# Optimization experiments

Measured on AMD Instinct MI355X. Metric: run time of the kernel, lower is better.

The kernel has to match this reference:

```python
import jax, jax.numpy as jnp
import numpy as np

N = 50000   # nodes
E = 800000  # edges
H = 128     # hidden_dim
K = 4       # Chebyshev order
EPS_BN = 1e-5
EPS_L2 = 1e-12


def setup_inputs() -> dict:
    key = jax.random.key(0)
    ks = jax.random.split(key, 8)
    x = jax.random.normal(ks[0], (N, 3), dtype=jnp.float32)
    edge_index = jax.random.randint(ks[1], (2, E), 0, N, dtype=jnp.int32)

    def lin(k, fi, fo):
        s = 1.0 / np.sqrt(fi)
        return jax.random.uniform(k, (fi, fo), jnp.float32, -s, s)

    def cheb_params(k, fi, fo):
        kk = jax.random.split(k, K)
        W = jnp.stack([lin(kk[i], fi, fo) for i in range(K)])  # [K, fi, fo]
        b = jnp.zeros((fo,), jnp.float32)
        return W, b

    W1, b1 = cheb_params(ks[2], 3, H)
    W2, b2 = cheb_params(ks[3], H, H)
    W3, b3 = cheb_params(ks[4], H, H)
    W4, b4 = cheb_params(ks[5], H, H)
    Wr = lin(ks[6], H, 3)
    br = jnp.zeros((3,), jnp.float32)
    ones = jnp.ones((H,), jnp.float32)
    zeros = jnp.zeros((H,), jnp.float32)
    return {
        'x': x, 'edge_index': edge_index,
        'W1': W1, 'b1': b1, 'W2': W2, 'b2': b2,
        'W3': W3, 'b3': b3, 'W4': W4, 'b4': b4,
        'g1': ones, 'be1': zeros, 'g2': ones, 'be2': zeros,
        'g3': ones, 'be3': zeros, 'Wr': Wr, 'br': br,
    }


def _prop(h, src, dst, norm):
    # one sparse Laplacian application: out[dst] += norm * h[src]
    return jax.ops.segment_sum(norm[:, None] * h[src], dst, num_segments=N)


def _cheb(h, src, dst, norm, W, b):
    # PyG ChebConv with sym normalization, lambda_max=2 -> L_hat edge weights
    # are -D^-1/2 A D^-1/2 with zero diagonal (encoded in norm).
    out = h @ W[0]
    Tx0, Tx1 = h, _prop(h, src, dst, norm)
    out = out + Tx1 @ W[1]
    for k in range(2, W.shape[0]):
        Tx2 = 2.0 * _prop(Tx1, src, dst, norm) - Tx0
        out = out + Tx2 @ W[k]
        Tx0, Tx1 = Tx1, Tx2
    return out + b


def _bn(h, g, b):
    # BatchNorm1d in training mode: batch stats over node dim, biased var
    m = h.mean(axis=0)
    v = h.var(axis=0)
    return g * (h - m) * jax.lax.rsqrt(v + EPS_BN) + b


def reference(x, edge_index, W1, b1, W2, b2, W3, b3, W4, b4,
              g1, be1, g2, be2, g3, be3, Wr, br):
    src, dst = edge_index[0], edge_index[1]
    deg = jax.ops.segment_sum(jnp.ones((E,), jnp.float32), src, num_segments=N)
    dinv = jnp.where(deg > 0, jax.lax.rsqrt(jnp.maximum(deg, 1.0)), 0.0)
    norm = -dinv[src] * dinv[dst]

    h = _bn(jax.nn.leaky_relu(_cheb(x, src, dst, norm, W1, b1)), g1, be1)
    h = _bn(jax.nn.leaky_relu(_cheb(h, src, dst, norm, W2, b2)), g2, be2)
    h = _bn(jax.nn.relu(_cheb(h, src, dst, norm, W3, b3)), g3, be3)
    h = _cheb(h, src, dst, norm, W4, b4)
    # F.normalize(p=2, dim=1)
    h = h / jnp.maximum(jnp.linalg.norm(h, axis=1, keepdims=True), EPS_L2)
    return h @ Wr + br
```

## Files before the change

### kernel.cpp

```cpp
#include <hip/hip_runtime.h>
#include <hip/hip_fp16.h>

#define HD 128

typedef __attribute__((ext_vector_type(8))) short bf16x8;
typedef __attribute__((ext_vector_type(4))) float f32x4;
typedef unsigned int u32;

struct h4s { __half2 a, b; };

__device__ __forceinline__ float lrelu(float x, float s) { return x > 0.f ? x : s * x; }

__device__ __forceinline__ u32 bf16rtne(float x) {
  u32 u = __float_as_uint(x);
  return (u + 0x7fffu + ((u >> 16) & 1u)) >> 16;
}

__global__ void k_edge_count(const int* __restrict__ src, const int* __restrict__ dst,
                             int* __restrict__ degc, int* __restrict__ cnt,
                             int* __restrict__ ledge, int E) {
  int e = blockIdx.x * blockDim.x + threadIdx.x;
  if (e < E) {
    atomicAdd(&degc[src[e]], 1);
    ledge[e] = atomicAdd(&cnt[dst[e]], 1);
  }
}

__global__ __launch_bounds__(1024) void k_scan1(const int* __restrict__ cnt,
                                                int* __restrict__ rowptr,
                                                int* __restrict__ bsums, int n) {
  __shared__ int buf[1024];
  int i = blockIdx.x * 1024 + threadIdx.x;
  int v = (i < n) ? cnt[i] : 0;
  buf[threadIdx.x] = v;
  __syncthreads();
  for (int o = 1; o < 1024; o <<= 1) {
    int t = (threadIdx.x >= (unsigned)o) ? buf[threadIdx.x - o] : 0;
    __syncthreads();
    buf[threadIdx.x] += t;
    __syncthreads();
  }
  if (i < n) rowptr[i] = buf[threadIdx.x] - v;
  if (threadIdx.x == 1023) bsums[blockIdx.x] = buf[1023];
}

__global__ __launch_bounds__(1024) void k_scan3(int* __restrict__ rowptr,
                                                const int* __restrict__ bsums,
                                                const int* __restrict__ degc,
                                                float* __restrict__ dinv, int n, int Etot,
                                                int nb) {
  __shared__ int blockoff;
  if (nb <= 64) {
    if (threadIdx.x < 64) {
      int lane = threadIdx.x;
      int v = (lane < nb) ? bsums[lane] : 0;
      int inc = v;
#pragma unroll
      for (int o = 1; o < 64; o <<= 1) {
        int t = __shfl_up(inc, o, 64);
        if (lane >= o) inc += t;
      }
      if (lane == (int)blockIdx.x) blockoff = inc - v;
    }
  } else if (threadIdx.x == 0) {
    int sum = 0;
    for (int t = 0; t < (int)blockIdx.x; ++t) sum += bsums[t];
    blockoff = sum;
  }
  __syncthreads();
  int i = blockIdx.x * 1024 + threadIdx.x;
  if (i < n) {
    rowptr[i] += blockoff;
    int dg = degc[i];
    dinv[i] = dg > 0 ? rsqrtf((float)dg) : 0.f;
  }
  if (i == 0) rowptr[n] = Etot;
}

__global__ void k_fill(const int* __restrict__ src, const int* __restrict__ dst,
                       const int* __restrict__ ledge, const int* __restrict__ rowptr,
                       const float* __restrict__ dinv, uint2* __restrict__ cw, int E) {
  int e = blockIdx.x * blockDim.x + threadIdx.x;
  if (e < E) {
    int s = src[e], d = dst[e];
    int p = rowptr[d] + ledge[e];
    cw[p] = make_uint2((u32)s, __float_as_uint(-dinv[s] * dinv[d]));
  }
}

__global__ void k_prop3(const int* __restrict__ rowptr, const uint2* __restrict__ cw,
                        const float* __restrict__ Hs, const float* __restrict__ Sub,
                        float* __restrict__ Out, float scale, int n) {
  int r = blockIdx.x * blockDim.x + threadIdx.x;
  if (r >= n) return;
  int b = rowptr[r], e = rowptr[r + 1];
  float a0 = 0.f, a1 = 0.f, a2 = 0.f;
  for (int j = b; j < e; ++j) {
    uint2 m = cw[j];
    int s = (int)m.x;
    float w = __uint_as_float(m.y);
    a0 = fmaf(w, Hs[s * 3 + 0], a0);
    a1 = fmaf(w, Hs[s * 3 + 1], a1);
    a2 = fmaf(w, Hs[s * 3 + 2], a2);
  }
  float r0 = scale * a0, r1 = scale * a1, r2 = scale * a2;
  if (Sub) { r0 -= Sub[r * 3 + 0]; r1 -= Sub[r * 3 + 1]; r2 -= Sub[r * 3 + 2]; }
  Out[r * 3 + 0] = r0; Out[r * 3 + 1] = r1; Out[r * 3 + 2] = r2;
}

template <int PHI>
__global__ __launch_bounds__(256) void k_prop128(
    const int* __restrict__ rowptr, const uint2* __restrict__ cw,
    const __half* __restrict__ Ph, const __half* __restrict__ Sub,
    __half* __restrict__ Outh, float scale, int n,
    const float* __restrict__ gsc, const float* __restrict__ gsh,
    const float* __restrict__ ssc, const float* __restrict__ ssh, float slope) {
  int r = blockIdx.x * 4 + (int)(threadIdx.x >> 6);
  int lane = threadIdx.x & 63;
  if (r >= n) return;
  int b = rowptr[r], e = rowptr[r + 1];
  int fl = (lane & 31) << 2;
  int half = lane >> 5;
  float ax = 0.f, ay = 0.f, az = 0.f, aw = 0.f, ws = 0.f;
  int j = b;
  for (; j + 7 < e; j += 8) {
    h4s h[4];
    float w[4];
#pragma unroll
    for (int q = 0; q < 4; ++q) {
      int idx = j + 2 * q + half;
      uint2 m = cw[idx];
      w[q] = __uint_as_float(m.y);
      h[q] = *(const h4s*)&Ph[(size_t)m.x * HD + fl];
    }
#pragma unroll
    for (int q = 0; q < 4; ++q) {
      float2 f0 = __half22float2(h[q].a);
      float2 f1 = __half22float2(h[q].b);
      if (PHI) {
        f0.x = lrelu(f0.x, slope); f0.y = lrelu(f0.y, slope);
        f1.x = lrelu(f1.x, slope); f1.y = lrelu(f1.y, slope);
        ws += w[q];
      }
      ax = fmaf(w[q], f0.x, ax);
      ay = fmaf(w[q], f0.y, ay);
      az = fmaf(w[q], f1.x, az);
      aw = fmaf(w[q], f1.y, aw);
    }
  }
  for (; j + 1 < e; j += 2) {
    int idx = j + half;
    uint2 m = cw[idx];
    float w = __uint_as_float(m.y);
    h4s h = *(const h4s*)&Ph[(size_t)m.x * HD + fl];
    float2 f0 = __half22float2(h.a);
    float2 f1 = __half22float2(h.b);
    if (PHI) {
      f0.x = lrelu(f0.x, slope); f0.y = lrelu(f0.y, slope);
      f1.x = lrelu(f1.x, slope); f1.y = lrelu(f1.y, slope);
      ws += w;
    }
    ax = fmaf(w, f0.x, ax);
    ay = fmaf(w, f0.y, ay);
    az = fmaf(w, f1.x, az);
    aw = fmaf(w, f1.y, aw);
  }
  if (j < e && half == 0) {
    uint2 m = cw[j];
    float w = __uint_as_float(m.y);
    h4s h = *(const h4s*)&Ph[(size_t)m.x * HD + fl];
    float2 f0 = __half22float2(h.a);
    float2 f1 = __half22float2(h.b);
    if (PHI) {
      f0.x = lrelu(f0.x, slope); f0.y = lrelu(f0.y, slope);
      f1.x = lrelu(f1.x, slope); f1.y = lrelu(f1.y, slope);
      ws += w;
    }
    ax = fmaf(w, f0.x, ax);
    ay = fmaf(w, f0.y, ay);
    az = fmaf(w, f1.x, az);
    aw = fmaf(w, f1.y, aw);
  }
  ax += __shfl_xor(ax, 32, 64);
  ay += __shfl_xor(ay, 32, 64);
  az += __shfl_xor(az, 32, 64);
  aw += __shfl_xor(aw, 32, 64);
  if (PHI) {
    ws += __shfl_xor(ws, 32, 64);
    float4 g4 = *(const float4*)&gsc[fl];
    float4 s4 = *(const float4*)&gsh[fl];
    ax = fmaf(ax, g4.x, ws * s4.x);
    ay = fmaf(ay, g4.y, ws * s4.y);
    az = fmaf(az, g4.z, ws * s4.z);
    aw = fmaf(aw, g4.w, ws * s4.w);
  }
  float4 o = make_float4(scale * ax, scale * ay, scale * az, scale * aw);
  if (Sub) {
    h4s sh4 = *(const h4s*)&Sub[(size_t)r * HD + fl];
    float2 s0 = __half22float2(sh4.a);
    float2 s1 = __half22float2(sh4.b);
    if (ssc != nullptr) {
      float4 c4 = *(const float4*)&ssc[fl];
      float4 d4 = *(const float4*)&ssh[fl];
      s0.x = fmaf(lrelu(s0.x, slope), c4.x, d4.x);
      s0.y = fmaf(lrelu(s0.y, slope), c4.y, d4.y);
      s1.x = fmaf(lrelu(s1.x, slope), c4.z, d4.z);
      s1.y = fmaf(lrelu(s1.y, slope), c4.w, d4.w);
    }
    o.x -= s0.x; o.y -= s0.y; o.z -= s1.x; o.w -= s1.y;
  }
  if (half == 0) {
    h4s ho;
    ho.a = __float22half2_rn(make_float2(o.x, o.y));
    ho.b = __float22half2_rn(make_float2(o.z, o.w));
    *(h4s*)&Outh[(size_t)r * HD + fl] = ho;
  }
}

__global__ __launch_bounds__(128) void k_l1gemm(
    const float* __restrict__ X, const float* __restrict__ T1, const float* __restrict__ T2,
    const float* __restrict__ T3, const float* __restrict__ W1, const float* __restrict__ b1,
    __half* __restrict__ Outh, float* __restrict__ bnsum, float* __restrict__ bnsq,
    float slope, int n, int rpb) {
  int j = threadIdx.x;
  float w[12];
#pragma unroll
  for (int t = 0; t < 4; ++t)
#pragma unroll
    for (int c = 0; c < 3; ++c) w[t * 3 + c] = W1[(t * 3 + c) * HD + j];
  float bj = b1[j];
  int r0 = blockIdx.x * rpb, r1 = min(r0 + rpb, n);
  float s = 0.f, q = 0.f;
  for (int r = r0; r < r1; ++r) {
    float acc = bj;
#pragma unroll
    for (int c = 0; c < 3; ++c) {
      acc = fmaf(X [r * 3 + c], w[0 + c], acc);
      acc = fmaf(T1[r * 3 + c], w[3 + c], acc);
      acc = fmaf(T2[r * 3 + c], w[6 + c], acc);
      acc = fmaf(T3[r * 3 + c], w[9 + c], acc);
    }
    Outh[(size_t)r * HD + j] = __float2half(acc);
    float a = lrelu(acc, slope);
    s += a;
    q = fmaf(a, a, q);
  }
  atomicAdd(&bnsum[j], s);
  atomicAdd(&bnsq[j], q);
}

__global__ void k_wsplit3(const float* __restrict__ W2, const float* __restrict__ W3,
                          const float* __restrict__ W4, uint4* __restrict__ Whi,
                          uint4* __restrict__ Wlo) {
  int flat = blockIdx.x * 256 + threadIdx.x;
  int wsel = flat >> 13;
  int f = flat & 8191;
  const float* W = (wsel == 0) ? W2 : (wsel == 1) ? W3 : W4;
  int n = f & 127, K8 = f >> 7;
  int chunk = K8 >> 2, g = K8 & 3;
  bf16x8 hv, lv;
#pragma unroll
  for (int i = 0; i < 8; ++i) {
    int k = chunk * 32 + ((i >> 2) << 4) + g * 4 + (i & 3);
    float v = W[(size_t)k * HD + n];
    u32 hb = bf16rtne(v);
    float hf = __uint_as_float(hb << 16);
    u32 lb = bf16rtne(v - hf);
    hv[i] = (short)hb;
    lv[i] = (short)lb;
  }
  int slot = chunk * 512 + (n >> 4) * 64 + g * 16 + (n & 15);
  Whi[wsel * 8192 + slot] = *(uint4*)&hv;
  Wlo[wsel * 8192 + slot] = *(uint4*)&lv;
}

__global__ __launch_bounds__(256) void k_gemm4m(
    const __half* __restrict__ T0, const __half* __restrict__ T1,
    const __half* __restrict__ T2, const __half* __restrict__ T3,
    const uint4* __restrict__ Whi, const uint4* __restrict__ Wlo,
    const float* __restrict__ bias, __half* __restrict__ OUTh,
    float* bnsum, float* bnsq, float stat_slope,
    const float* __restrict__ gsc, const float* __restrict__ gsh, float phi_slope,
    int nrows) {
  __shared__ short sAh[2048], sAl[2048];
  __shared__ short sWh[4096], sWl[4096];
  __shared__ float redS[128], redQ[128];

  int tid = threadIdx.x;
  int lane = tid & 63, w = tid >> 6, wr = w >> 1, wc = w & 1;
  int g = (tid >> 4) & 3;
  int ri = tid & 15;
  int row0 = blockIdx.x * 64;
  int arow = row0 + w * 16 + ri;
  bool aval = arow < nrows;

  f32x4 zero = {0.f, 0.f, 0.f, 0.f};
  f32x4 acc[2][4];
#pragma unroll
  for (int mi = 0; mi < 2; ++mi)
#pragma unroll
    for (int nj = 0; nj < 4; ++nj) acc[mi][nj] = zero;

  if (tid < 128) { redS[tid] = 0.f; redQ[tid] = 0.f; }

  for (int chunk = 0; chunk < 16; ++chunk) {
    const __half* Ts = (chunk < 4) ? T0 : (chunk < 8) ? T1 : (chunk < 12) ? T2 : T3;
    int kc = chunk & 3;
    float vals[8] = {0.f, 0.f, 0.f, 0.f, 0.f, 0.f, 0.f, 0.f};
    if (aval) {
      const __half* ap = Ts + (size_t)arow * HD + kc * 32 + g * 4;
      h4s va = *(const h4s*)ap;
      h4s vb = *(const h4s*)(ap + 16);
      float2 f0 = __half22float2(va.a), f1 = __half22float2(va.b);
      float2 f2 = __half22float2(vb.a), f3 = __half22float2(vb.b);
      vals[0] = f0.x; vals[1] = f0.y; vals[2] = f1.x; vals[3] = f1.y;
      vals[4] = f2.x; vals[5] = f2.y; vals[6] = f3.x; vals[7] = f3.y;
    }
    size_t wbase = (size_t)chunk * 512;
    uint4 wh0 = Whi[wbase + tid], wh1 = Whi[wbase + 256 + tid];
    uint4 wl0 = Wlo[wbase + tid], wl1 = Wlo[wbase + 256 + tid];

    __syncthreads();

    if (gsc != nullptr && chunk < 4) {
#pragma unroll
      for (int i = 0; i < 8; ++i) {
        int f = kc * 32 + g * 4 + (i & 3) + ((i >> 2) << 4);
        vals[i] = fmaf(lrelu(vals[i], phi_slope), gsc[f], gsh[f]);
      }
    }
    bf16x8 hv, lv;
#pragma unroll
    for (int i = 0; i < 8; ++i) {
      u32 hb = bf16rtne(vals[i]);
      float hf = __uint_as_float(hb << 16);
      u32 lb = bf16rtne(vals[i] - hf);
      hv[i] = (short)hb;
      lv[i] = (short)lb;
    }
    *(bf16x8*)&sAh[tid * 8] = hv;
    *(bf16x8*)&sAl[tid * 8] = lv;
    *(uint4*)&sWh[tid * 8] = wh0;
    *(uint4*)&sWh[(256 + tid) * 8] = wh1;
    *(uint4*)&sWl[tid * 8] = wl0;
    *(uint4*)&sWl[(256 + tid) * 8] = wl1;
    __syncthreads();

    bf16x8 ah[2], al[2], bh[4], bl[4];
#pragma unroll
    for (int mi = 0; mi < 2; ++mi) {
      ah[mi] = *(const bf16x8*)&sAh[((wr * 2 + mi) * 64 + lane) * 8];
      al[mi] = *(const bf16x8*)&sAl[((wr * 2 + mi) * 64 + lane) * 8];
    }
#pragma unroll
    for (int nj = 0; nj < 4; ++nj) {
      bh[nj] = *(const bf16x8*)&sWh[((wc * 4 + nj) * 64 + lane) * 8];
      bl[nj] = *(const bf16x8*)&sWl[((wc * 4 + nj) * 64 + lane) * 8];
    }
#pragma unroll
    for (int mi = 0; mi < 2; ++mi)
#pragma unroll
      for (int nj = 0; nj < 4; ++nj) {
        acc[mi][nj] = __builtin_amdgcn_mfma_f32_16x16x32_bf16(ah[mi], bh[nj], acc[mi][nj], 0, 0, 0);
        acc[mi][nj] = __builtin_amdgcn_mfma_f32_16x16x32_bf16(ah[mi], bl[nj], acc[mi][nj], 0, 0, 0);
        acc[mi][nj] = __builtin_amdgcn_mfma_f32_16x16x32_bf16(al[mi], bh[nj], acc[mi][nj], 0, 0, 0);
      }
  }

  int l4 = (lane >> 4) * 4, ni = lane & 15;
  bool stats = (bnsum != nullptr);
#pragma unroll
  for (int nj = 0; nj < 4; ++nj) {
    int c = wc * 64 + nj * 16 + ni;
    float bcol = bias[c];
    float s = 0.f, q = 0.f;
#pragma unroll
    for (int mi = 0; mi < 2; ++mi)
#pragma unroll
      for (int j = 0; j < 4; ++j) {
        int row = row0 + (wr * 2 + mi) * 16 + l4 + j;
        if (row < nrows) {
          float v = acc[mi][nj][j] + bcol;
          OUTh[(size_t)row * HD + c] = __float2half(v);
          if (stats) {
            float a = lrelu(v, stat_slope);
            s += a;
            q = fmaf(a, a, q);
          }
        }
      }
    if (stats) {
      s += __shfl_xor(s, 16, 64);
      s += __shfl_xor(s, 32, 64);
      q += __shfl_xor(q, 16, 64);
      q += __shfl_xor(q, 32, 64);
      if (lane < 16) {
        atomicAdd(&redS[c], s);
        atomicAdd(&redQ[c], q);
      }
    }
  }
  if (stats) {
    __syncthreads();
    if (tid < 128) {
      atomicAdd(&bnsum[tid], redS[tid]);
      atomicAdd(&bnsq[tid], redQ[tid]);
    }
  }
}

__global__ void k_bnfin(const float* __restrict__ bsum, const float* __restrict__ bsq,
                        const float* __restrict__ g, const float* __restrict__ be,
                        float* __restrict__ scaleb, float* __restrict__ shiftb, int n) {
  int f = threadIdx.x;
  if (f < HD) {
    float m = bsum[f] / (float)n;
    float v = bsq[f] / (float)n - m * m;
    float rs = rsqrtf(v + 1e-5f);
    float sc = g[f] * rs;
    scaleb[f] = sc;
    shiftb[f] = be[f] - m * sc;
  }
}

__global__ __launch_bounds__(256) void k_final(const __half* __restrict__ Hb,
                                               const float* __restrict__ Wr,
                                               const float* __restrict__ br,
                                               float* __restrict__ out, int n) {
  int r = blockIdx.x * 4 + (int)(threadIdx.x >> 6);
  int lane = threadIdx.x & 63;
  if (r >= n) return;
  float h0 = __half2float(Hb[(size_t)r * HD + lane]);
  float h1 = __half2float(Hb[(size_t)r * HD + 64 + lane]);
  float ss = h0 * h0 + h1 * h1;
#pragma unroll
  for (int o = 32; o; o >>= 1) ss += __shfl_xor(ss, o, 64);
  float inv = 1.f / fmaxf(sqrtf(ss), 1e-12f);
  h0 *= inv; h1 *= inv;
  float o0 = h0 * Wr[lane * 3 + 0] + h1 * Wr[(64 + lane) * 3 + 0];
  float o1 = h0 * Wr[lane * 3 + 1] + h1 * Wr[(64 + lane) * 3 + 1];
  float o2 = h0 * Wr[lane * 3 + 2] + h1 * Wr[(64 + lane) * 3 + 2];
#pragma unroll
  for (int o = 32; o; o >>= 1) {
    o0 += __shfl_xor(o0, o, 64);
    o1 += __shfl_xor(o1, o, 64);
    o2 += __shfl_xor(o2, o, 64);
  }
  if (lane == 0) {
    out[r * 3 + 0] = o0 + br[0];
    out[r * 3 + 1] = o1 + br[1];
    out[r * 3 + 2] = o2 + br[2];
  }
}

extern "C" void kernel_launch(void* const* d_in, const int* in_sizes, int n_in,
                              void* d_out, int out_size, void* d_ws, size_t ws_size,
                              hipStream_t stream) {
  const float* x  = (const float*)d_in[0];
  const int*   ei = (const int*)d_in[1];
  const float* W1 = (const float*)d_in[2];
  const float* b1 = (const float*)d_in[3];
  const float* W2 = (const float*)d_in[4];
  const float* b2 = (const float*)d_in[5];
  const float* W3 = (const float*)d_in[6];
  const float* b3 = (const float*)d_in[7];
  const float* W4 = (const float*)d_in[8];
  const float* b4 = (const float*)d_in[9];
  const float* g1 = (const float*)d_in[10];
  const float* be1= (const float*)d_in[11];
  const float* g2 = (const float*)d_in[12];
  const float* be2= (const float*)d_in[13];
  const float* g3 = (const float*)d_in[14];
  const float* be3= (const float*)d_in[15];
  const float* Wr = (const float*)d_in[16];
  const float* br = (const float*)d_in[17];

  const int N = in_sizes[0] / 3;
  const int E = in_sizes[1] / 2;
  const int* src = ei;
  const int* dst = ei + E;
  float* out = (float*)d_out;

  char* wp = (char*)d_ws;
  size_t used = 0;
  auto alloc = [&](size_t bytes) -> void* {
    void* p = (void*)(wp + used);
    used += (bytes + 255) & ~(size_t)255;
    return p;
  };
  int*   deg2   = (int*)alloc((size_t)2 * N * 4);
  int*   rowptr = (int*)alloc((size_t)(N + 1) * 4);
  float* dinv   = (float*)alloc((size_t)N * 4);
  int*   bsums  = (int*)alloc(256 * 4);
  int*   ledge  = (int*)alloc((size_t)E * 4);
  uint2* cw     = (uint2*)alloc((size_t)E * 8);
  float* t1     = (float*)alloc((size_t)N * 3 * 4);
  float* t2     = (float*)alloc((size_t)N * 3 * 4);
  float* t3     = (float*)alloc((size_t)N * 3 * 4);
  __half* phA   = (__half*)alloc((size_t)N * HD * 2);
  __half* phB   = (__half*)alloc((size_t)N * HD * 2);
  __half* phC   = (__half*)alloc((size_t)N * HD * 2);
  __half* phD   = (__half*)alloc((size_t)N * HD * 2);
  float* stats  = (float*)alloc(6 * HD * 4);
  float* scsh   = (float*)alloc(6 * HD * 4);
  uint4* Whi3   = (uint4*)alloc(3 * 8192 * 16);
  uint4* Wlo3   = (uint4*)alloc(3 * 8192 * 16);
  if (used > ws_size) return;

  int* degc = deg2;
  int* cnt  = deg2 + N;
  float* bnsum1 = stats + 0 * HD; float* bnsq1 = stats + 1 * HD;
  float* bnsum2 = stats + 2 * HD; float* bnsq2 = stats + 3 * HD;
  float* bnsum3 = stats + 4 * HD; float* bnsq3 = stats + 5 * HD;
  float* sc1 = scsh + 0 * HD; float* sh1 = scsh + 1 * HD;
  float* sc2 = scsh + 2 * HD; float* sh2 = scsh + 3 * HD;
  float* sc3 = scsh + 4 * HD; float* sh3 = scsh + 5 * HD;

  const int eb = (E + 255) / 256;
  const int nb = (N + 255) / 256;
  const int pb = (N + 3) / 4;
  const int sb = (N + 1023) / 1024;
  const int gbm = (N + 63) / 64;

  hipMemsetAsync(stats, 0, 6 * HD * 4, stream);
  hipMemsetAsync(deg2, 0, (size_t)2 * N * 4, stream);
  k_edge_count<<<eb, 256, 0, stream>>>(src, dst, degc, cnt, ledge, E);
  k_scan1<<<sb, 1024, 0, stream>>>(cnt, rowptr, bsums, N);
  k_scan3<<<sb, 1024, 0, stream>>>(rowptr, bsums, degc, dinv, N, E, sb);
  k_fill<<<eb, 256, 0, stream>>>(src, dst, ledge, rowptr, dinv, cw, E);
  k_wsplit3<<<96, 256, 0, stream>>>(W2, W3, W4, Whi3, Wlo3);

  k_prop3<<<nb, 256, 0, stream>>>(rowptr, cw, x, nullptr, t1, 1.f, N);
  k_prop3<<<nb, 256, 0, stream>>>(rowptr, cw, t1, x, t2, 2.f, N);
  k_prop3<<<nb, 256, 0, stream>>>(rowptr, cw, t2, t1, t3, 2.f, N);
  k_l1gemm<<<(N + 255) / 256, 128, 0, stream>>>(x, t1, t2, t3, W1, b1, phA,
                                                bnsum1, bnsq1, 0.01f, N, 256);
  k_bnfin<<<1, 128, 0, stream>>>(bnsum1, bnsq1, g1, be1, sc1, sh1, N);

  auto cheb_layer = [&](const uint4* Whi, const uint4* Wlo, const float* bk,
                        const float* psc, const float* psh, float phi_slope,
                        float* bs, float* bq, float stat_slope) {
    k_prop128<1><<<pb, 256, 0, stream>>>(rowptr, cw, phA, nullptr, phB, 1.f, N,
                                         psc, psh, nullptr, nullptr, phi_slope);
    k_prop128<0><<<pb, 256, 0, stream>>>(rowptr, cw, phB, phA, phC, 2.f, N,
                                         nullptr, nullptr, psc, psh, phi_slope);
    k_prop128<0><<<pb, 256, 0, stream>>>(rowptr, cw, phC, phB, phD, 2.f, N,
                                         nullptr, nullptr, nullptr, nullptr, 0.f);
    k_gemm4m<<<gbm, 256, 0, stream>>>(phA, phB, phC, phD, Whi, Wlo, bk, phA,
                                      bs, bq, stat_slope, psc, psh, phi_slope, N);
  };

  cheb_layer(Whi3, Wlo3, b2, sc1, sh1, 0.01f, bnsum2, bnsq2, 0.01f);
  k_bnfin<<<1, 128, 0, stream>>>(bnsum2, bnsq2, g2, be2, sc2, sh2, N);
  cheb_layer(Whi3 + 8192, Wlo3 + 8192, b3, sc2, sh2, 0.01f, bnsum3, bnsq3, 0.0f);
  k_bnfin<<<1, 128, 0, stream>>>(bnsum3, bnsq3, g3, be3, sc3, sh3, N);
  cheb_layer(Whi3 + 16384, Wlo3 + 16384, b4, sc3, sh3, 0.0f, nullptr, nullptr, 0.0f);

  k_final<<<pb, 256, 0, stream>>>(phA, Wr, br, out, N);
}
```

Before: 684.8 us.

## Split hidden features into 32-wide column panels and use fp16 split-weight MFMA

Stores all 128-wide hidden activations in four column-major panels of 32 features each. Each SpMM propagation now runs as four passes, one per panel, so the gathered working set per pass (N×32 halfs) is small enough to stay resident in cache, with eight edges processed per wavefront. Separately, the GEMM switches from a three-term bf16 hi/lo split to fp16 activations with hi/lo fp16 weights, dropping one MFMA per tile and the activation split. The cost is four times as many propagation launches and rereads of the CSR structure, plus some precision risk from fp16 weight splitting.

```diff
diff --git a/kernel.cpp b/kernel.cpp
--- a/kernel.cpp
+++ b/kernel.cpp
@@ -3,18 +3,13 @@
 
 #define HD 128
 
-typedef __attribute__((ext_vector_type(8))) short bf16x8;
+typedef __attribute__((ext_vector_type(8))) _Float16 f16x8;
 typedef __attribute__((ext_vector_type(4))) float f32x4;
 typedef unsigned int u32;
 
 struct h4s { __half2 a, b; };
 
 __device__ __forceinline__ float lrelu(float x, float s) { return x > 0.f ? x : s * x; }
-
-__device__ __forceinline__ u32 bf16rtne(float x) {
-  u32 u = __float_as_uint(x);
-  return (u + 0x7fffu + ((u >> 16) & 1u)) >> 16;
-}
 
 __global__ void k_edge_count(const int* __restrict__ src, const int* __restrict__ dst,
                              int* __restrict__ degc, int* __restrict__ cnt,
@@ -111,48 +106,24 @@
 template <int PHI>
 __global__ __launch_bounds__(256) void k_prop128(
     const int* __restrict__ rowptr, const uint2* __restrict__ cw,
-    const __half* __restrict__ Ph, const __half* __restrict__ Sub,
-    __half* __restrict__ Outh, float scale, int n,
+    const __half* __restrict__ PhC, const __half* __restrict__ SubC,
+    __half* __restrict__ OutC, float scale, int n, int pass,
     const float* __restrict__ gsc, const float* __restrict__ gsh,
     const float* __restrict__ ssc, const float* __restrict__ ssh, float slope) {
   int r = blockIdx.x * 4 + (int)(threadIdx.x >> 6);
   int lane = threadIdx.x & 63;
   if (r >= n) return;
   int b = rowptr[r], e = rowptr[r + 1];
-  int fl = (lane & 31) << 2;
-  int half = lane >> 5;
-  float ax = 0.f, ay = 0.f, az = 0.f, aw = 0.f, ws = 0.f;
-  int j = b;
-  for (; j + 7 < e; j += 8) {
-    h4s h[4];
-    float w[4];
-#pragma unroll
-    for (int q = 0; q < 4; ++q) {
-      int idx = j + 2 * q + half;
-      uint2 m = cw[idx];
-      w[q] = __uint_as_float(m.y);
-      h[q] = *(const h4s*)&Ph[(size_t)m.x * HD + fl];
-    }
-#pragma unroll
-    for (int q = 0; q < 4; ++q) {
-      float2 f0 = __half22float2(h[q].a);
-      float2 f1 = __half22float2(h[q].b);
-      if (PHI) {
-        f0.x = lrelu(f0.x, slope); f0.y = lrelu(f0.y, slope);
-        f1.x = lrelu(f1.x, slope); f1.y = lrelu(f1.y, slope);
-        ws += w[q];
-      }
-      ax = fmaf(w[q], f0.x, ax);
-      ay = fmaf(w[q], f0.y, ay);
-      az = fmaf(w[q], f1.x, az);
-      aw = fmaf(w[q], f1.y, aw);
-    }
-  }
-  for (; j + 1 < e; j += 2) {
-    int idx = j + half;
-    uint2 m = cw[idx];
+  int eo = lane >> 3;
+  int fo = (lane & 7) << 2;
+  const __half* src = PhC + (size_t)pass * n * 32;
+  float a0 = 0.f, a1 = 0.f, a2 = 0.f, a3 = 0.f, ws = 0.f;
+  for (int j = b; j < e; j += 8) {
+    int idx = j + eo;
+    bool v = idx < e;
+    uint2 m = v ? cw[idx] : make_uint2(0u, 0u);
     float w = __uint_as_float(m.y);
-    h4s h = *(const h4s*)&Ph[(size_t)m.x * HD + fl];
+    h4s h = *(const h4s*)&src[(size_t)m.x * 32 + fo];
     float2 f0 = __half22float2(h.a);
     float2 f1 = __half22float2(h.b);
     if (PHI) {
@@ -160,67 +131,55 @@
       f1.x = lrelu(f1.x, slope); f1.y = lrelu(f1.y, slope);
       ws += w;
     }
-    ax = fmaf(w, f0.x, ax);
-    ay = fmaf(w, f0.y, ay);
-    az = fmaf(w, f1.x, az);
-    aw = fmaf(w, f1.y, aw);
-  }
-  if (j < e && half == 0) {
-    uint2 m = cw[j];
-    float w = __uint_as_float(m.y);
-    h4s h = *(const h4s*)&Ph[(size_t)m.x * HD + fl];
-    float2 f0 = __half22float2(h.a);
-    float2 f1 = __half22float2(h.b);
+    a0 = fmaf(w, f0.x, a0);
+    a1 = fmaf(w, f0.y, a1);
+    a2 = fmaf(w, f1.x, a2);
+    a3 = fmaf(w, f1.y, a3);
+  }
+#pragma unroll
+  for (int mk = 8; mk <= 32; mk <<= 1) {
+    a0 += __shfl_xor(a0, mk, 64);
+    a1 += __shfl_xor(a1, mk, 64);
+    a2 += __shfl_xor(a2, mk, 64);
+    a3 += __shfl_xor(a3, mk, 64);
+    if (PHI) ws += __shfl_xor(ws, mk, 64);
+  }
+  if (eo == 0) {
+    int fg = pass * 32 + fo;
     if (PHI) {
-      f0.x = lrelu(f0.x, slope); f0.y = lrelu(f0.y, slope);
-      f1.x = lrelu(f1.x, slope); f1.y = lrelu(f1.y, slope);
-      ws += w;
-    }
-    ax = fmaf(w, f0.x, ax);
-    ay = fmaf(w, f0.y, ay);
-    az = fmaf(w, f1.x, az);
-    aw = fmaf(w, f1.y, aw);
-  }
-  ax += __shfl_xor(ax, 32, 64);
-  ay += __shfl_xor(ay, 32, 64);
-  az += __shfl_xor(az, 32, 64);
-  aw += __shfl_xor(aw, 32, 64);
-  if (PHI) {
-    ws += __shfl_xor(ws, 32, 64);
-    float4 g4 = *(const float4*)&gsc[fl];
-    float4 s4 = *(const float4*)&gsh[fl];
-    ax = fmaf(ax, g4.x, ws * s4.x);
-    ay = fmaf(ay, g4.y, ws * s4.y);
-    az = fmaf(az, g4.z, ws * s4.z);
-    aw = fmaf(aw, g4.w, ws * s4.w);
-  }
-  float4 o = make_float4(scale * ax, scale * ay, scale * az, scale * aw);
-  if (Sub) {
-    h4s sh4 = *(const h4s*)&Sub[(size_t)r * HD + fl];
-    float2 s0 = __half22float2(sh4.a);
-    float2 s1 = __half22float2(sh4.b);
-    if (ssc != nullptr) {
-      float4 c4 = *(const float4*)&ssc[fl];
-      float4 d4 = *(const float4*)&ssh[fl];
-      s0.x = fmaf(lrelu(s0.x, slope), c4.x, d4.x);
-      s0.y = fmaf(lrelu(s0.y, slope), c4.y, d4.y);
-      s1.x = fmaf(lrelu(s1.x, slope), c4.z, d4.z);
-      s1.y = fmaf(lrelu(s1.y, slope), c4.w, d4.w);
-    }
-    o.x -= s0.x; o.y -= s0.y; o.z -= s1.x; o.w -= s1.y;
-  }
-  if (half == 0) {
+      float4 g4 = *(const float4*)&gsc[fg];
+      float4 s4 = *(const float4*)&gsh[fg];
+      a0 = fmaf(a0, g4.x, ws * s4.x);
+      a1 = fmaf(a1, g4.y, ws * s4.y);
+      a2 = fmaf(a2, g4.z, ws * s4.z);
+      a3 = fmaf(a3, g4.w, ws * s4.w);
+    }
+    float4 o = make_float4(scale * a0, scale * a1, scale * a2, scale * a3);
+    if (SubC) {
+      h4s sh4 = *(const h4s*)&SubC[(size_t)pass * n * 32 + (size_t)r * 32 + fo];
+      float2 s0 = __half22float2(sh4.a);
+      float2 s1 = __half22float2(sh4.b);
+      if (ssc != nullptr) {
+        float4 c4 = *(const float4*)&ssc[fg];
+        float4 d4 = *(const float4*)&ssh[fg];
+        s0.x = fmaf(lrelu(s0.x, slope), c4.x, d4.x);
+        s0.y = fmaf(lrelu(s0.y, slope), c4.y, d4.y);
+        s1.x = fmaf(lrelu(s1.x, slope), c4.z, d4.z);
+        s1.y = fmaf(lrelu(s1.y, slope), c4.w, d4.w);
+      }
+      o.x -= s0.x; o.y -= s0.y; o.z -= s1.x; o.w -= s1.y;
+    }
     h4s ho;
     ho.a = __float22half2_rn(make_float2(o.x, o.y));
     ho.b = __float22half2_rn(make_float2(o.z, o.w));
-    *(h4s*)&Outh[(size_t)r * HD + fl] = ho;
+    *(h4s*)&OutC[(size_t)pass * n * 32 + (size_t)r * 32 + fo] = ho;
   }
 }
 
 __global__ __launch_bounds__(128) void k_l1gemm(
     const float* __restrict__ X, const float* __restrict__ T1, const float* __restrict__ T2,
     const float* __restrict__ T3, const float* __restrict__ W1, const float* __restrict__ b1,
-    __half* __restrict__ Outh, float* __restrict__ bnsum, float* __restrict__ bnsq,
+    __half* __restrict__ OutC, float* __restrict__ bnsum, float* __restrict__ bnsq,
     float slope, int n, int rpb) {
   int j = threadIdx.x;
   float w[12];
@@ -229,6 +188,7 @@
 #pragma unroll
     for (int c = 0; c < 3; ++c) w[t * 3 + c] = W1[(t * 3 + c) * HD + j];
   float bj = b1[j];
+  size_t obase = (size_t)(j >> 5) * n * 32 + (j & 31);
   int r0 = blockIdx.x * rpb, r1 = min(r0 + rpb, n);
   float s = 0.f, q = 0.f;
   for (int r = r0; r < r1; ++r) {
@@ -240,7 +200,7 @@
       acc = fmaf(T2[r * 3 + c], w[6 + c], acc);
       acc = fmaf(T3[r * 3 + c], w[9 + c], acc);
     }
-    Outh[(size_t)r * HD + j] = __float2half(acc);
+    OutC[obase + (size_t)r * 32] = __float2half(acc);
     float a = lrelu(acc, slope);
     s += a;
     q = fmaf(a, a, q);
@@ -258,16 +218,15 @@
   const float* W = (wsel == 0) ? W2 : (wsel == 1) ? W3 : W4;
   int n = f & 127, K8 = f >> 7;
   int chunk = K8 >> 2, g = K8 & 3;
-  bf16x8 hv, lv;
+  f16x8 hv, lv;
 #pragma unroll
   for (int i = 0; i < 8; ++i) {
     int k = chunk * 32 + ((i >> 2) << 4) + g * 4 + (i & 3);
     float v = W[(size_t)k * HD + n];
-    u32 hb = bf16rtne(v);
-    float hf = __uint_as_float(hb << 16);
-    u32 lb = bf16rtne(v - hf);
-    hv[i] = (short)hb;
-    lv[i] = (short)lb;
+    _Float16 hh = (_Float16)v;
+    _Float16 hl = (_Float16)(v - (float)hh);
+    hv[i] = hh;
+    lv[i] = hl;
   }
   int slot = chunk * 512 + (n >> 4) * 64 + g * 16 + (n & 15);
   Whi[wsel * 8192 + slot] = *(uint4*)&hv;
@@ -282,8 +241,8 @@
     float* bnsum, float* bnsq, float stat_slope,
     const float* __restrict__ gsc, const float* __restrict__ gsh, float phi_slope,
     int nrows) {
-  __shared__ short sAh[2048], sAl[2048];
-  __shared__ short sWh[4096], sWl[4096];
+  __shared__ __half sA[2048];
+  __shared__ __half sWh[4096], sWl[4096];
   __shared__ float redS[128], redQ[128];
 
   int tid = threadIdx.x;
@@ -306,15 +265,13 @@
   for (int chunk = 0; chunk < 16; ++chunk) {
     const __half* Ts = (chunk < 4) ? T0 : (chunk < 8) ? T1 : (chunk < 12) ? T2 : T3;
     int kc = chunk & 3;
-    float vals[8] = {0.f, 0.f, 0.f, 0.f, 0.f, 0.f, 0.f, 0.f};
+    h4s va, vb;
+    *(uint2*)&va = make_uint2(0u, 0u);
+    *(uint2*)&vb = make_uint2(0u, 0u);
     if (aval) {
-      const __half* ap = Ts + (size_t)arow * HD + kc * 32 + g * 4;
-      h4s va = *(const h4s*)ap;
-      h4s vb = *(const h4s*)(ap + 16);
-      float2 f0 = __half22float2(va.a), f1 = __half22float2(va.b);
-      float2 f2 = __half22float2(vb.a), f3 = __half22float2(vb.b);
-      vals[0] = f0.x; vals[1] = f0.y; vals[2] = f1.x; vals[3] = f1.y;
-      vals[4] = f2.x; vals[5] = f2.y; vals[6] = f3.x; vals[7] = f3.y;
+      const __half* ap = Ts + ((size_t)kc * nrows + arow) * 32 + g * 4;
+      va = *(const h4s*)ap;
+      vb = *(const h4s*)(ap + 16);
     }
     size_t wbase = (size_t)chunk * 512;
     uint4 wh0 = Whi[wbase + tid], wh1 = Whi[wbase + 256 + tid];
@@ -323,47 +280,44 @@
     __syncthreads();
 
     if (gsc != nullptr && chunk < 4) {
+      float fv[8];
+      float2 f0 = __half22float2(va.a), f1 = __half22float2(va.b);
+      float2 f2 = __half22float2(vb.a), f3 = __half22float2(vb.b);
+      fv[0] = f0.x; fv[1] = f0.y; fv[2] = f1.x; fv[3] = f1.y;
+      fv[4] = f2.x; fv[5] = f2.y; fv[6] = f3.x; fv[7] = f3.y;
 #pragma unroll
       for (int i = 0; i < 8; ++i) {
         int f = kc * 32 + g * 4 + (i & 3) + ((i >> 2) << 4);
-        vals[i] = fmaf(lrelu(vals[i], phi_slope), gsc[f], gsh[f]);
+        fv[i] = fmaf(lrelu(fv[i], phi_slope), gsc[f], gsh[f]);
       }
-    }
-    bf16x8 hv, lv;
-#pragma unroll
-    for (int i = 0; i < 8; ++i) {
-      u32 hb = bf16rtne(vals[i]);
-      float hf = __uint_as_float(hb << 16);
-      u32 lb = bf16rtne(vals[i] - hf);
-      hv[i] = (short)hb;
-      lv[i] = (short)lb;
-    }
-    *(bf16x8*)&sAh[tid * 8] = hv;
-    *(bf16x8*)&sAl[tid * 8] = lv;
+      va.a = __float22half2_rn(make_float2(fv[0], fv[1]));
+      va.b = __float22half2_rn(make_float2(fv[2], fv[3]));
+      vb.a = __float22half2_rn(make_float2(fv[4], fv[5]));
+      vb.b = __float22half2_rn(make_float2(fv[6], fv[7]));
+    }
+    *(h4s*)&sA[tid * 8] = va;
+    *(h4s*)&sA[tid * 8 + 4] = vb;
     *(uint4*)&sWh[tid * 8] = wh0;
     *(uint4*)&sWh[(256 + tid) * 8] = wh1;
     *(uint4*)&sWl[tid * 8] = wl0;
     *(uint4*)&sWl[(256 + tid) * 8] = wl1;
     __syncthreads();
 
-    bf16x8 ah[2], al[2], bh[4], bl[4];
-#pragma unroll
-    for (int mi = 0; mi < 2; ++mi) {
-      ah[mi] = *(const bf16x8*)&sAh[((wr * 2 + mi) * 64 + lane) * 8];
-      al[mi] = *(const bf16x8*)&sAl[((wr * 2 + mi) * 64 + lane) * 8];
-    }
+    f16x8 a[2], bh[4], bl[4];
+#pragma unroll
+    for (int mi = 0; mi < 2; ++mi)
+      a[mi] = *(const f16x8*)&sA[((wr * 2 + mi) * 64 + lane) * 8];
 #pragma unroll
     for (int nj = 0; nj < 4; ++nj) {
-      bh[nj] = *(const bf16x8*)&sWh[((wc * 4 + nj) * 64 + lane) * 8];
-      bl[nj] = *(const bf16x8*)&sWl[((wc * 4 + nj) * 64 + lane) * 8];
+      bh[nj] = *(const f16x8*)&sWh[((wc * 4 + nj) * 64 + lane) * 8];
+      bl[nj] = *(const f16x8*)&sWl[((wc * 4 + nj) * 64 + lane) * 8];
     }
 #pragma unroll
     for (int mi = 0; mi < 2; ++mi)
 #pragma unroll
       for (int nj = 0; nj < 4; ++nj) {
-        acc[mi][nj] = __builtin_amdgcn_mfma_f32_16x16x32_bf16(ah[mi], bh[nj], acc[mi][nj], 0, 0, 0);
-        acc[mi][nj] = __builtin_amdgcn_mfma_f32_16x16x32_bf16(ah[mi], bl[nj], acc[mi][nj], 0, 0, 0);
-        acc[mi][nj] = __builtin_amdgcn_mfma_f32_16x16x32_bf16(al[mi], bh[nj], acc[mi][nj], 0, 0, 0);
+        acc[mi][nj] = __builtin_amdgcn_mfma_f32_16x16x32_f16(a[mi], bh[nj], acc[mi][nj], 0, 0, 0);
+        acc[mi][nj] = __builtin_amdgcn_mfma_f32_16x16x32_f16(a[mi], bl[nj], acc[mi][nj], 0, 0, 0);
       }
   }
 
@@ -373,6 +327,7 @@
   for (int nj = 0; nj < 4; ++nj) {
     int c = wc * 64 + nj * 16 + ni;
     float bcol = bias[c];
+    size_t obase = (size_t)(c >> 5) * nrows * 32 + (c & 31);
     float s = 0.f, q = 0.f;
 #pragma unroll
     for (int mi = 0; mi < 2; ++mi)
@@ -381,7 +336,7 @@
         int row = row0 + (wr * 2 + mi) * 16 + l4 + j;
         if (row < nrows) {
           float v = acc[mi][nj][j] + bcol;
-          OUTh[(size_t)row * HD + c] = __float2half(v);
+          OUTh[obase + (size_t)row * 32] = __float2half(v);
           if (stats) {
             float a = lrelu(v, stat_slope);
             s += a;
@@ -423,15 +378,15 @@
   }
 }
 
-__global__ __launch_bounds__(256) void k_final(const __half* __restrict__ Hb,
+__global__ __launch_bounds__(256) void k_final(const __half* __restrict__ HbC,
                                                const float* __restrict__ Wr,
                                                const float* __restrict__ br,
                                                float* __restrict__ out, int n) {
   int r = blockIdx.x * 4 + (int)(threadIdx.x >> 6);
   int lane = threadIdx.x & 63;
   if (r >= n) return;
-  float h0 = __half2float(Hb[(size_t)r * HD + lane]);
-  float h1 = __half2float(Hb[(size_t)r * HD + 64 + lane]);
+  float h0 = __half2float(HbC[((size_t)(lane >> 5) * n + r) * 32 + (lane & 31)]);
+  float h1 = __half2float(HbC[((size_t)(2 + (lane >> 5)) * n + r) * 32 + (lane & 31)]);
   float ss = h0 * h0 + h1 * h1;
 #pragma unroll
   for (int o = 32; o; o >>= 1) ss += __shfl_xor(ss, o, 64);
@@ -540,12 +495,15 @@
   auto cheb_layer = [&](const uint4* Whi, const uint4* Wlo, const float* bk,
                         const float* psc, const float* psh, float phi_slope,
                         float* bs, float* bq, float stat_slope) {
-    k_prop128<1><<<pb, 256, 0, stream>>>(rowptr, cw, phA, nullptr, phB, 1.f, N,
-                                         psc, psh, nullptr, nullptr, phi_slope);
-    k_prop128<0><<<pb, 256, 0, stream>>>(rowptr, cw, phB, phA, phC, 2.f, N,
-                                         nullptr, nullptr, psc, psh, phi_slope);
-    k_prop128<0><<<pb, 256, 0, stream>>>(rowptr, cw, phC, phB, phD, 2.f, N,
-                                         nullptr, nullptr, nullptr, nullptr, 0.f);
+    for (int p = 0; p < 4; ++p)
+      k_prop128<1><<<pb, 256, 0, stream>>>(rowptr, cw, phA, nullptr, phB, 1.f, N, p,
+                                           psc, psh, nullptr, nullptr, phi_slope);
+    for (int p = 0; p < 4; ++p)
+      k_prop128<0><<<pb, 256, 0, stream>>>(rowptr, cw, phB, phA, phC, 2.f, N, p,
+                                           nullptr, nullptr, psc, psh, phi_slope);
+    for (int p = 0; p < 4; ++p)
+      k_prop128<0><<<pb, 256, 0, stream>>>(rowptr, cw, phC, phB, phD, 2.f, N, p,
+                                           nullptr, nullptr, nullptr, nullptr, 0.f);
     k_gemm4m<<<gbm, 256, 0, stream>>>(phA, phB, phC, phD, Whi, Wlo, bk, phA,
                                       bs, bq, stat_slope, psc, psh, phi_slope, N);
   };
```

Measured after the change: 1.154 ms. 68.5% more time.
